# Performance work log

Hardware: AMD Instinct MI355X
Metric: run time of the kernel (lower is better)

## Reference

```python
import jax, jax.numpy as jnp
import numpy as np

N_NODES = 100000
N_EDGES = 1250000
IN_CH = 64
HID = 64
OUT = 64


def setup_inputs() -> dict:
    key = jax.random.key(0)
    ks = jax.random.split(key, 8)
    x = jax.random.normal(ks[0], (N_NODES, IN_CH), dtype=jnp.float32)
    edge_index = jax.random.randint(ks[1], (2, N_EDGES), 0, N_NODES, dtype=jnp.int64)
    # glorot-ish init for weights, zeros for biases (PyG GCNConv default-style)
    def glorot(k, fan_in, fan_out):
        s = (6.0 / (fan_in + fan_out)) ** 0.5
        return jax.random.uniform(k, (fan_in, fan_out), jnp.float32, -s, s)
    W1 = glorot(ks[2], IN_CH, HID)
    b1 = jnp.zeros((HID,), jnp.float32)
    W2 = glorot(ks[3], HID, HID)
    b2 = jnp.zeros((HID,), jnp.float32)
    W3 = glorot(ks[4], HID, OUT)
    b3 = jnp.zeros((OUT,), jnp.float32)
    return {"x": x, "edge_index": edge_index, "W1": W1, "b1": b1,
            "W2": W2, "b2": b2, "W3": W3, "b3": b3}


def _gcn_conv(x, src, dst, W, b, n_nodes):
    """PyG GCNConv: out = D^{-1/2} (A + I) D^{-1/2} (x W) + b.
    src/dst already include self-loops."""
    deg = jax.ops.segment_sum(jnp.ones_like(dst, dtype=x.dtype), dst,
                              num_segments=n_nodes)  # in-degree incl. self-loop
    dinv = jnp.where(deg > 0, jax.lax.rsqrt(deg), 0.0)
    norm = dinv[src] * dinv[dst]                       # [E+N]
    h = x @ W                                          # [N, F_out] small GEMM
    msg = h[src] * norm[:, None]                       # gather + scale (edge-wise)
    out = jax.ops.segment_sum(msg, dst, num_segments=n_nodes)  # scatter-add
    return out + b


def reference(x, edge_index, W1, b1, W2, b2, W3, b3):
    n_nodes = x.shape[0]
    loop = jnp.arange(n_nodes, dtype=edge_index.dtype)
    src = jnp.concatenate([edge_index[0], loop])  # messages flow src -> dst
    dst = jnp.concatenate([edge_index[1], loop])
    h = jax.nn.relu(_gcn_conv(x, src, dst, W1, b1, n_nodes))
    h = jax.nn.relu(_gcn_conv(h, src, dst, W2, b2, n_nodes))
    return h @ W3 + b3
```

## Files before the change

### kernel.cpp

```cpp
#include <hip/hip_runtime.h>
#include <hip/hip_bf16.h>


#define WG 256
#define BSHIFT 9
#define BSIZE  (1 << BSHIFT)
#define BCAP   8192
#define PCHUNK 2048
#define WT_LD  72

typedef __attribute__((ext_vector_type(8))) short bf16x8;
typedef __attribute__((ext_vector_type(4))) float f32x4;

__device__ __forceinline__ unsigned short f2bf(float f) {
    union { float f; unsigned u; } v; v.f = f;
    unsigned r = v.u + 0x7fffu + ((v.u >> 16) & 1u);
    return (unsigned short)(r >> 16);
}
__device__ __forceinline__ float bf2f(unsigned short h) {
    union { unsigned u; float f; } v; v.u = ((unsigned)h) << 16;
    return v.f;
}

__global__ __launch_bounds__(WG) void bcur_init(int* __restrict__ cur2, int nbk) {
    int b = threadIdx.x;
    if (b < nbk) cur2[b] = b * BCAP;
}

__global__ __launch_bounds__(WG) void partition(const int* __restrict__ ei,
                                                int* __restrict__ cur2,
                                                unsigned long long* __restrict__ pairs,
                                                int E) {
    __shared__ int hist[256];
    __shared__ int gbase[256];
    __shared__ int lb[256];
    __shared__ int wsum4[4];
    __shared__ unsigned long long sp[PCHUNK];
    __shared__ int sd[PCHUNK];
    const int t = threadIdx.x;
    const int lane = t & 63;
    const int w = t >> 6;
    const int base = blockIdx.x * PCHUNK;
    const int total = min(PCHUNK, E - base);

    hist[t] = 0;
    __syncthreads();

    int s[8], d[8], r[8];
#pragma unroll
    for (int i = 0; i < 8; i++) {
        int e = base + i * WG + t;
        bool ok = e < E;
        s[i] = ok ? ei[e] : 0;
        d[i] = ok ? ei[E + e] : 0;
        r[i] = ok ? atomicAdd(&hist[d[i] >> BSHIFT], 1) : 0;
        if (!ok) d[i] = -1;
    }
    __syncthreads();

    int hv = hist[t];
    if (hv > 0) gbase[t] = atomicAdd(&cur2[t], hv);
    int sc = hv;
#pragma unroll
    for (int ofs = 1; ofs < 64; ofs <<= 1) {
        int u = __shfl_up(sc, ofs);
        if (lane >= ofs) sc += u;
    }
    if (lane == 63) wsum4[w] = sc;
    __syncthreads();
    if (t == 0) {
        int run = 0;
#pragma unroll
        for (int i = 0; i < 4; i++) { int x = wsum4[i]; wsum4[i] = run; run += x; }
    }
    __syncthreads();
    lb[t] = sc + wsum4[w] - hv;
    __syncthreads();

#pragma unroll
    for (int i = 0; i < 8; i++) {
        if (d[i] >= 0) {
            int b = d[i] >> BSHIFT;
            int slot = lb[b] + r[i];
            sp[slot] = ((unsigned long long)(unsigned)(d[i] & (BSIZE - 1)) << 32) |
                       (unsigned)s[i];
            sd[slot] = gbase[b] + r[i];
        }
    }
    __syncthreads();

    for (int j = t; j < total; j += WG)
        pairs[sd[j]] = sp[j];
}

__global__ __launch_bounds__(WG) void bsum_scan(const int* __restrict__ cur2,
                                                int* __restrict__ bbase, int nbk,
                                                int* __restrict__ off, int N) {
    __shared__ int sums[WG];
    const int t = threadIdx.x;
    int s = (t < nbk) ? (cur2[t] - t * BCAP) : 0;
    sums[t] = s;
    __syncthreads();
    for (int ofs = 1; ofs < WG; ofs <<= 1) {
        int u = (t >= ofs) ? sums[t - ofs] : 0;
        __syncthreads();
        sums[t] += u;
        __syncthreads();
    }
    if (t < nbk) bbase[t] = sums[t] - s;
    if (t == WG - 1) off[N] = sums[WG - 1];
}

__global__ __launch_bounds__(1024) void csr_local(const unsigned long long* __restrict__ pairs,
                                                  const int* __restrict__ cur2,
                                                  const int* __restrict__ bbase,
                                                  int* __restrict__ off,
                                                  float* __restrict__ dinv,
                                                  int* __restrict__ csr, int N) {
    __shared__ unsigned long long sp[BCAP];
    __shared__ int cs[BCAP];
    __shared__ int h[BSIZE];
    __shared__ int cur[BSIZE];
    __shared__ int wsum[8];
    const int b = blockIdx.x;
    const int t = threadIdx.x;
    const int lane = t & 63;
    const int w = t >> 6;
    const int node0 = b << BSHIFT;
    const int nlocal = min(BSIZE, N - node0);
    const int pstart = b * BCAP;
    const int cnt = cur2[b] - pstart;
    const int base = bbase[b];

    if (t < BSIZE) h[t] = 0;
    __syncthreads();

    for (int e = t; e < cnt; e += 1024) {
        unsigned long long p = pairs[pstart + e];
        sp[e] = p;
        atomicAdd(&h[(int)(p >> 32)], 1);
    }
    __syncthreads();

    int myh = (t < BSIZE) ? h[t] : 0;
    int s = myh;
#pragma unroll
    for (int d = 1; d < 64; d <<= 1) {
        int u = __shfl_up(s, d);
        if (lane >= d) s += u;
    }
    if (t < BSIZE && lane == 63) wsum[w] = s;
    __syncthreads();
    if (t == 0) {
        int run = 0;
#pragma unroll
        for (int i = 0; i < 8; i++) { int x = wsum[i]; wsum[i] = run; run += x; }
    }
    __syncthreads();
    if (t < BSIZE) {
        int excl = s + wsum[w] - myh;
        cur[t] = excl;
        if (t < nlocal) {
            off[node0 + t] = base + excl;
            dinv[node0 + t] = rsqrtf((float)(myh + 1));
        }
    }
    __syncthreads();

    for (int e = t; e < cnt; e += 1024) {
        unsigned long long p = sp[e];
        int pos = atomicAdd(&cur[(int)(p >> 32)], 1);
        cs[pos] = (int)(p & 0xffffffffu);
    }
    __syncthreads();

    for (int j = t; j < cnt; j += 1024)
        csr[base + j] = cs[j];
}

__global__ __launch_bounds__(WG, 4) void gemm_fused(
    const float* __restrict__ in, const float* __restrict__ W,
    const float* __restrict__ dinv, const float* __restrict__ b_pre, int pre_flag,
    int post_scale, const float* __restrict__ b_post,
    void* __restrict__ out1, int out_bf16, int n_rows)
{
    __shared__ __align__(16) short Wh[64 * WT_LD];
    __shared__ __align__(16) short Wl[64 * WT_LD];

    const int t = threadIdx.x;

    const float4* W4 = (const float4*)W;
#pragma unroll
    for (int i = 0; i < 4; i++) {
        int q = i * WG + t;
        float4 w = W4[q];
        int base = q * 4;
        int k = base >> 6;
        int j0 = base & 63;
        float wf[4] = {w.x, w.y, w.z, w.w};
#pragma unroll
        for (int e = 0; e < 4; e++) {
            unsigned short h = f2bf(wf[e]);
            Wh[(j0 + e) * WT_LD + k] = (short)h;
            Wl[(j0 + e) * WT_LD + k] = (short)f2bf(wf[e] - bf2f(h));
        }
    }

    const int wid = t >> 6;
    const int l = t & 63;
    const int lr = l & 15;
    const int lk = l >> 4;
    const int row0 = blockIdx.x * 64 + wid * 16;
    const int arow = row0 + lr;
    const int srow = (arow < n_rows) ? arow : 0;

    bf16x8 ah[2], al[2];
    float dv = pre_flag ? dinv[srow] : 0.f;
#pragma unroll
    for (int kc = 0; kc < 2; kc++) {
        const float* p = in + (size_t)srow * 64 + kc * 32 + lk * 8;
        float4 v0 = *(const float4*)p;
        float4 v1 = *(const float4*)(p + 4);
        float vv[8] = {v0.x, v0.y, v0.z, v0.w, v1.x, v1.y, v1.z, v1.w};
        if (pre_flag) {
            const float* bp = b_pre + kc * 32 + lk * 8;
            float4 b0 = *(const float4*)bp;
            float4 b1 = *(const float4*)(bp + 4);
            float bb[8] = {b0.x, b0.y, b0.z, b0.w, b1.x, b1.y, b1.z, b1.w};
#pragma unroll
            for (int e = 0; e < 8; e++)
                vv[e] = fmaxf(fmaf(dv, vv[e], bb[e]), 0.f);
        }
#pragma unroll
        for (int e = 0; e < 8; e++) {
            unsigned short h = f2bf(vv[e]);
            ah[kc][e] = (short)h;
            al[kc][e] = (short)f2bf(vv[e] - bf2f(h));
        }
    }

    __syncthreads();

    f32x4 acc[4] = {};
#pragma unroll
    for (int ct = 0; ct < 4; ct++) {
#pragma unroll
        for (int kc = 0; kc < 2; kc++) {
            const short* ph = &Wh[(ct * 16 + lr) * WT_LD + kc * 32 + lk * 8];
            const short* pl = &Wl[(ct * 16 + lr) * WT_LD + kc * 32 + lk * 8];
            bf16x8 bh = *(const bf16x8*)ph;
            bf16x8 bl = *(const bf16x8*)pl;
            acc[ct] = __builtin_amdgcn_mfma_f32_16x16x32_bf16(ah[kc], bh, acc[ct], 0, 0, 0);
            acc[ct] = __builtin_amdgcn_mfma_f32_16x16x32_bf16(al[kc], bh, acc[ct], 0, 0, 0);
            acc[ct] = __builtin_amdgcn_mfma_f32_16x16x32_bf16(ah[kc], bl, acc[ct], 0, 0, 0);
            acc[ct] = __builtin_amdgcn_mfma_f32_16x16x32_bf16(al[kc], bl, acc[ct], 0, 0, 0);
        }
    }

#pragma unroll
    for (int r = 0; r < 4; r++) {
        int orow = row0 + lk * 4 + r;
        if (orow >= n_rows) continue;
        float sc = post_scale ? dinv[orow] : 1.0f;
#pragma unroll
        for (int ct = 0; ct < 4; ct++) {
            float bpv = b_post ? b_post[ct * 16 + lr] : 0.f;
            float o = fmaf(acc[ct][r], sc, bpv);
            if (out_bf16)
                ((unsigned short*)out1)[((size_t)orow << 6) + ct * 16 + lr] = f2bf(o);
            else
                ((float*)out1)[((size_t)orow << 6) + ct * 16 + lr] = o;
        }
    }
}

__device__ __forceinline__ void acc_bf16x2(float& a, float& b, unsigned u) {
    union { unsigned v; float f; } lo, hi;
    lo.v = u << 16;
    hi.v = u & 0xffff0000u;
    a += lo.f;
    b += hi.f;
}

__global__ __launch_bounds__(WG) void aggregate(
    const uint2* __restrict__ A4, float* __restrict__ B,
    const int* __restrict__ off, const int* __restrict__ csr, int N)
{
    const int t = threadIdx.x;
    const int l = t & 63;
    const int c = l & 15;
    const int g = l >> 4;
    const int gl = g << 4;
    int node = blockIdx.x * 16 + ((t >> 6) << 2) + g;
    const bool valid = node < N;
    if (!valid) node = N - 1;

    const int s0 = off[node];
    const int s1 = valid ? off[node + 1] : s0;

    uint2 v = A4[((size_t)node << 4) + c];
    float4 acc = make_float4(0.f, 0.f, 0.f, 0.f);
    acc_bf16x2(acc.x, acc.y, v.x);
    acc_bf16x2(acc.z, acc.w, v.y);

    for (int p = s0; p < s1; p += 16) {
        const int cnt = min(16, s1 - p);
        int idx = (c < cnt) ? csr[p + c] : 0;
#pragma unroll
        for (int k = 0; k < 16; k++) {
            int src = __shfl(idx, gl + k);
            if (k < cnt) {
                uint2 wv = A4[((size_t)src << 4) + c];
                acc_bf16x2(acc.x, acc.y, wv.x);
                acc_bf16x2(acc.z, acc.w, wv.y);
            }
        }
    }

    if (valid)
        *(float4*)(B + ((size_t)node << 6) + 4 * c) = acc;
}

extern "C" void kernel_launch(void* const* d_in, const int* in_sizes, int n_in,
                              void* d_out, int out_size, void* d_ws, size_t ws_size,
                              hipStream_t stream) {
    const float* x  = (const float*)d_in[0];
    const int*   ei = (const int*)d_in[1];
    const float* W1 = (const float*)d_in[2];
    const float* b1 = (const float*)d_in[3];
    const float* W2 = (const float*)d_in[4];
    const float* b2 = (const float*)d_in[5];
    const float* W3 = (const float*)d_in[6];
    const float* b3 = (const float*)d_in[7];
    float* out = (float*)d_out;

    const int N = in_sizes[0] / 64;
    const int E = in_sizes[1] / 2;
    const int nbk = (N + BSIZE - 1) / BSIZE;

    int*   off  = (int*)d_ws;
    int*   csr  = off + (N + 1);
    int*   cur2 = csr + E;
    int*   bbase= cur2 + 256;
    uintptr_t pa = (uintptr_t)(bbase + 256);
    pa = (pa + 255) & ~(uintptr_t)255;
    float* dinv = (float*)pa;
    __hip_bfloat16* A = (__hip_bfloat16*)(dinv + N);
    float* B    = (float*)(A + (size_t)N * 64);
    unsigned long long* pairs = (unsigned long long*)B;

    const int gG = (N + 63) / 64;
    const int gA = (N + 15) / 16;
    const int gP = (E + PCHUNK - 1) / PCHUNK;

    bcur_init<<<1,   WG, 0, stream>>>(cur2, nbk);
    partition<<<gP,  WG, 0, stream>>>(ei, cur2, pairs, E);
    bsum_scan<<<1,   WG, 0, stream>>>(cur2, bbase, nbk, off, N);
    csr_local<<<nbk, 1024, 0, stream>>>(pairs, cur2, bbase, off, dinv, csr, N);

    gemm_fused<<<gG, WG, 0, stream>>>(x, W1, dinv, nullptr, 0, 1, nullptr, A, 1, N);
    aggregate <<<gA, WG, 0, stream>>>((const uint2*)A, B, off, csr, N);

    gemm_fused<<<gG, WG, 0, stream>>>(B, W2, dinv, b1, 1, 1, nullptr, A, 1, N);
    aggregate <<<gA, WG, 0, stream>>>((const uint2*)A, B, off, csr, N);

    gemm_fused<<<gG, WG, 0, stream>>>(B, W3, dinv, b2, 1, 0, b3, out, 0, N);
}
```

Measured before the change: 232.8 us.

## Fuse neighbor aggregation with the following GEMM into one kernel

Replaces the separate aggregate kernel plus the next GEMM with a single agg_gemm kernel. Each 64-row block gathers its neighbor sums into shared memory, applies dinv scaling, bias and ReLU, then runs split-bf16 MFMA against W held in LDS. This removes the fp32 intermediate B round trip to global memory and two kernel launches. In exchange it uses more shared memory per block, which may lower occupancy, and each thread now handles four nodes in sequence.

```diff
diff --git a/kernel.cpp b/kernel.cpp
--- a/kernel.cpp
+++ b/kernel.cpp
@@ -8,6 +8,7 @@
 #define BCAP   8192
 #define PCHUNK 2048
 #define WT_LD  72
+#define XS_LD  68
 
 typedef __attribute__((ext_vector_type(8))) short bf16x8;
 typedef __attribute__((ext_vector_type(4))) float f32x4;
@@ -20,6 +21,13 @@
 __device__ __forceinline__ float bf2f(unsigned short h) {
     union { unsigned u; float f; } v; v.u = ((unsigned)h) << 16;
     return v.f;
+}
+__device__ __forceinline__ void acc_bf16x2(float& a, float& b, unsigned u) {
+    union { unsigned v; float f; } lo, hi;
+    lo.v = u << 16;
+    hi.v = u & 0xffff0000u;
+    a += lo.f;
+    b += hi.f;
 }
 
 __global__ __launch_bounds__(WG) void bcur_init(int* __restrict__ cur2, int nbk) {
@@ -274,51 +282,133 @@
     }
 }
 
-__device__ __forceinline__ void acc_bf16x2(float& a, float& b, unsigned u) {
-    union { unsigned v; float f; } lo, hi;
-    lo.v = u << 16;
-    hi.v = u & 0xffff0000u;
-    a += lo.f;
-    b += hi.f;
-}
-
-__global__ __launch_bounds__(WG) void aggregate(
-    const uint2* __restrict__ A4, float* __restrict__ B,
-    const int* __restrict__ off, const int* __restrict__ csr, int N)
+__global__ __launch_bounds__(WG, 4) void agg_gemm(
+    const uint2* __restrict__ A4, const float* __restrict__ W,
+    const float* __restrict__ dinv, const float* __restrict__ b_pre,
+    int post_scale, const float* __restrict__ b_post,
+    void* __restrict__ out1, int out_bf16,
+    const int* __restrict__ off, const int* __restrict__ csr, int n_rows)
 {
+    __shared__ __align__(16) short Wh[64 * WT_LD];
+    __shared__ __align__(16) short Wl[64 * WT_LD];
+    __shared__ __align__(16) float xs[64 * XS_LD];
+
     const int t = threadIdx.x;
+
+    const float4* W4 = (const float4*)W;
+#pragma unroll
+    for (int i = 0; i < 4; i++) {
+        int q = i * WG + t;
+        float4 w = W4[q];
+        int base = q * 4;
+        int k = base >> 6;
+        int j0 = base & 63;
+        float wf[4] = {w.x, w.y, w.z, w.w};
+#pragma unroll
+        for (int e = 0; e < 4; e++) {
+            unsigned short h = f2bf(wf[e]);
+            Wh[(j0 + e) * WT_LD + k] = (short)h;
+            Wl[(j0 + e) * WT_LD + k] = (short)f2bf(wf[e] - bf2f(h));
+        }
+    }
+
     const int l = t & 63;
     const int c = l & 15;
     const int g = l >> 4;
-    const int gl = g << 4;
-    int node = blockIdx.x * 16 + ((t >> 6) << 2) + g;
-    const bool valid = node < N;
-    if (!valid) node = N - 1;
-
-    const int s0 = off[node];
-    const int s1 = valid ? off[node + 1] : s0;
-
-    uint2 v = A4[((size_t)node << 4) + c];
-    float4 acc = make_float4(0.f, 0.f, 0.f, 0.f);
-    acc_bf16x2(acc.x, acc.y, v.x);
-    acc_bf16x2(acc.z, acc.w, v.y);
-
-    for (int p = s0; p < s1; p += 16) {
-        const int cnt = min(16, s1 - p);
-        int idx = (c < cnt) ? csr[p + c] : 0;
-#pragma unroll
-        for (int k = 0; k < 16; k++) {
-            int src = __shfl(idx, gl + k);
-            if (k < cnt) {
-                uint2 wv = A4[((size_t)src << 4) + c];
-                acc_bf16x2(acc.x, acc.y, wv.x);
-                acc_bf16x2(acc.z, acc.w, wv.y);
+    const int qid = (t >> 6) * 4 + g;
+    const int row0 = blockIdx.x * 64;
+    const float4 bb = *(const float4*)(b_pre + 4 * c);
+
+#pragma unroll
+    for (int i = 0; i < 4; i++) {
+        int rloc = qid * 4 + i;
+        int node = row0 + rloc;
+        bool valid = node < n_rows;
+        int nc = valid ? node : n_rows - 1;
+        int s0 = off[nc];
+        int s1 = valid ? off[nc + 1] : s0;
+
+        uint2 v = A4[((size_t)nc << 4) + c];
+        float4 acc = make_float4(0.f, 0.f, 0.f, 0.f);
+        acc_bf16x2(acc.x, acc.y, v.x);
+        acc_bf16x2(acc.z, acc.w, v.y);
+
+        for (int p = s0; p < s1; p += 16) {
+            const int cnt = min(16, s1 - p);
+            int idx = (c < cnt) ? csr[p + c] : 0;
+#pragma unroll
+            for (int k = 0; k < 16; k++) {
+                int src = __shfl(idx, (g << 4) + k);
+                if (k < cnt) {
+                    uint2 wv = A4[((size_t)src << 4) + c];
+                    acc_bf16x2(acc.x, acc.y, wv.x);
+                    acc_bf16x2(acc.z, acc.w, wv.y);
+                }
             }
         }
-    }
-
-    if (valid)
-        *(float4*)(B + ((size_t)node << 6) + 4 * c) = acc;
+
+        float dv = dinv[nc];
+        float4 o;
+        o.x = fmaxf(fmaf(dv, acc.x, bb.x), 0.f);
+        o.y = fmaxf(fmaf(dv, acc.y, bb.y), 0.f);
+        o.z = fmaxf(fmaf(dv, acc.z, bb.z), 0.f);
+        o.w = fmaxf(fmaf(dv, acc.w, bb.w), 0.f);
+        *(float4*)(xs + rloc * XS_LD + 4 * c) = o;
+    }
+
+    __syncthreads();
+
+    const int wid = t >> 6;
+    const int lr = l & 15;
+    const int lk = l >> 4;
+    const int rw0 = blockIdx.x * 64 + wid * 16;
+
+    bf16x8 ah[2], al[2];
+#pragma unroll
+    for (int kc = 0; kc < 2; kc++) {
+        const float* p = xs + (wid * 16 + lr) * XS_LD + kc * 32 + lk * 8;
+        float4 v0 = *(const float4*)p;
+        float4 v1 = *(const float4*)(p + 4);
+        float vv[8] = {v0.x, v0.y, v0.z, v0.w, v1.x, v1.y, v1.z, v1.w};
+#pragma unroll
+        for (int e = 0; e < 8; e++) {
+            unsigned short h = f2bf(vv[e]);
+            ah[kc][e] = (short)h;
+            al[kc][e] = (short)f2bf(vv[e] - bf2f(h));
+        }
+    }
+
+    f32x4 acc[4] = {};
+#pragma unroll
+    for (int ct = 0; ct < 4; ct++) {
+#pragma unroll
+        for (int kc = 0; kc < 2; kc++) {
+            const short* ph = &Wh[(ct * 16 + lr) * WT_LD + kc * 32 + lk * 8];
+            const short* pl = &Wl[(ct * 16 + lr) * WT_LD + kc * 32 + lk * 8];
+            bf16x8 bh = *(const bf16x8*)ph;
+            bf16x8 bl = *(const bf16x8*)pl;
+            acc[ct] = __builtin_amdgcn_mfma_f32_16x16x32_bf16(ah[kc], bh, acc[ct], 0, 0, 0);
+            acc[ct] = __builtin_amdgcn_mfma_f32_16x16x32_bf16(al[kc], bh, acc[ct], 0, 0, 0);
+            acc[ct] = __builtin_amdgcn_mfma_f32_16x16x32_bf16(ah[kc], bl, acc[ct], 0, 0, 0);
+            acc[ct] = __builtin_amdgcn_mfma_f32_16x16x32_bf16(al[kc], bl, acc[ct], 0, 0, 0);
+        }
+    }
+
+#pragma unroll
+    for (int r = 0; r < 4; r++) {
+        int orow = rw0 + lk * 4 + r;
+        if (orow >= n_rows) continue;
+        float sc = post_scale ? dinv[orow] : 1.0f;
+#pragma unroll
+        for (int ct = 0; ct < 4; ct++) {
+            float bpv = b_post ? b_post[ct * 16 + lr] : 0.f;
+            float o = fmaf(acc[ct][r], sc, bpv);
+            if (out_bf16)
+                ((unsigned short*)out1)[((size_t)orow << 6) + ct * 16 + lr] = f2bf(o);
+            else
+                ((float*)out1)[((size_t)orow << 6) + ct * 16 + lr] = o;
+        }
+    }
 }
 
 extern "C" void kernel_launch(void* const* d_in, const int* in_sizes, int n_in,
@@ -345,12 +435,11 @@
     uintptr_t pa = (uintptr_t)(bbase + 256);
     pa = (pa + 255) & ~(uintptr_t)255;
     float* dinv = (float*)pa;
-    __hip_bfloat16* A = (__hip_bfloat16*)(dinv + N);
-    float* B    = (float*)(A + (size_t)N * 64);
-    unsigned long long* pairs = (unsigned long long*)B;
+    __hip_bfloat16* A  = (__hip_bfloat16*)(dinv + N);
+    __hip_bfloat16* A2 = A + (size_t)N * 64;
+    unsigned long long* pairs = (unsigned long long*)A2;
 
     const int gG = (N + 63) / 64;
-    const int gA = (N + 15) / 16;
     const int gP = (E + PCHUNK - 1) / PCHUNK;
 
     bcur_init<<<1,   WG, 0, stream>>>(cur2, nbk);
@@ -359,10 +448,10 @@
     csr_local<<<nbk, 1024, 0, stream>>>(pairs, cur2, bbase, off, dinv, csr, N);
 
     gemm_fused<<<gG, WG, 0, stream>>>(x, W1, dinv, nullptr, 0, 1, nullptr, A, 1, N);
-    aggregate <<<gA, WG, 0, stream>>>((const uint2*)A, B, off, csr, N);
-
-    gemm_fused<<<gG, WG, 0, stream>>>(B, W2, dinv, b1, 1, 1, nullptr, A, 1, N);
-    aggregate <<<gA, WG, 0, stream>>>((const uint2*)A, B, off, csr, N);
-
-    gemm_fused<<<gG, WG, 0, stream>>>(B, W3, dinv, b2, 1, 0, b3, out, 0, N);
-}
+
+    agg_gemm<<<gG, WG, 0, stream>>>((const uint2*)A, W2, dinv, b1, 1, nullptr,
+                                    A2, 1, off, csr, N);
+
+    agg_gemm<<<gG, WG, 0, stream>>>((const uint2*)A2, W3, dinv, b2, 0, b3,
+                                    out, 0, off, csr, N);
+}
```

Result: slower. 283.3 us (+21.7%).

## Pack edge pairs to 32 bits, halve bucket size, widen aggregate loads

Applied to the files above, without the earlier changes.

The CSR build now packs each (local dst, src) pair into one 32-bit word (src in 17 bits) instead of 64 bits. Buckets shrink to 256 nodes with 4096 capacity across up to 512 buckets, and the scans and csr_local block size are adjusted to match. The aggregate kernel moves from 16 lanes × 8 bytes per node row to 8 lanes × 16 bytes, with 32 neighbor indices staged per iteration. This is meant to cut pair-buffer traffic and LDS use and to use wider gathers. In exchange, node ids must fit in 17 bits, and a bucket overflows if a block of 256 nodes receives more than 4096 edges.

```diff
diff --git a/kernel.cpp b/kernel.cpp
--- a/kernel.cpp
+++ b/kernel.cpp
@@ -3,9 +3,10 @@
 
 
 #define WG 256
-#define BSHIFT 9
+#define BSHIFT 8
 #define BSIZE  (1 << BSHIFT)
-#define BCAP   8192
+#define NBK_MAX 512
+#define BCAP   4096
 #define PCHUNK 2048
 #define WT_LD  72
 
@@ -21,21 +22,28 @@
     union { unsigned u; float f; } v; v.u = ((unsigned)h) << 16;
     return v.f;
 }
-
-__global__ __launch_bounds__(WG) void bcur_init(int* __restrict__ cur2, int nbk) {
+__device__ __forceinline__ void acc_bf16x2(float& a, float& b, unsigned u) {
+    union { unsigned v; float f; } lo, hi;
+    lo.v = u << 16;
+    hi.v = u & 0xffff0000u;
+    a += lo.f;
+    b += hi.f;
+}
+
+__global__ __launch_bounds__(512) void bcur_init(int* __restrict__ cur2) {
     int b = threadIdx.x;
-    if (b < nbk) cur2[b] = b * BCAP;
+    cur2[b] = b * BCAP;
 }
 
 __global__ __launch_bounds__(WG) void partition(const int* __restrict__ ei,
                                                 int* __restrict__ cur2,
-                                                unsigned long long* __restrict__ pairs,
+                                                unsigned* __restrict__ pairs,
                                                 int E) {
-    __shared__ int hist[256];
-    __shared__ int gbase[256];
-    __shared__ int lb[256];
+    __shared__ int hist[NBK_MAX];
+    __shared__ int gbase[NBK_MAX];
+    __shared__ int lb[NBK_MAX];
     __shared__ int wsum4[4];
-    __shared__ unsigned long long sp[PCHUNK];
+    __shared__ unsigned sp[PCHUNK];
     __shared__ int sd[PCHUNK];
     const int t = threadIdx.x;
     const int lane = t & 63;
@@ -44,6 +52,7 @@
     const int total = min(PCHUNK, E - base);
 
     hist[t] = 0;
+    hist[t + 256] = 0;
     __syncthreads();
 
     int s[8], d[8], r[8];
@@ -58,9 +67,15 @@
     }
     __syncthreads();
 
-    int hv = hist[t];
-    if (hv > 0) gbase[t] = atomicAdd(&cur2[t], hv);
-    int sc = hv;
+    int hv0 = hist[t];
+    int hv1 = hist[t + 256];
+    if (hv0 > 0) gbase[t] = atomicAdd(&cur2[t], hv0);
+    if (hv1 > 0) gbase[t + 256] = atomicAdd(&cur2[t + 256], hv1);
+
+    int a0 = hist[2 * t];
+    int a1 = hist[2 * t + 1];
+    int ps = a0 + a1;
+    int sc = ps;
 #pragma unroll
     for (int ofs = 1; ofs < 64; ofs <<= 1) {
         int u = __shfl_up(sc, ofs);
@@ -74,7 +89,9 @@
         for (int i = 0; i < 4; i++) { int x = wsum4[i]; wsum4[i] = run; run += x; }
     }
     __syncthreads();
-    lb[t] = sc + wsum4[w] - hv;
+    int excl = sc + wsum4[w] - ps;
+    lb[2 * t] = excl;
+    lb[2 * t + 1] = excl + a0;
     __syncthreads();
 
 #pragma unroll
@@ -82,8 +99,7 @@
         if (d[i] >= 0) {
             int b = d[i] >> BSHIFT;
             int slot = lb[b] + r[i];
-            sp[slot] = ((unsigned long long)(unsigned)(d[i] & (BSIZE - 1)) << 32) |
-                       (unsigned)s[i];
+            sp[slot] = ((unsigned)(d[i] & (BSIZE - 1)) << 17) | (unsigned)s[i];
             sd[slot] = gbase[b] + r[i];
         }
     }
@@ -93,35 +109,43 @@
         pairs[sd[j]] = sp[j];
 }
 
-__global__ __launch_bounds__(WG) void bsum_scan(const int* __restrict__ cur2,
-                                                int* __restrict__ bbase, int nbk,
-                                                int* __restrict__ off, int N) {
-    __shared__ int sums[WG];
-    const int t = threadIdx.x;
+__global__ __launch_bounds__(512) void bsum_scan(const int* __restrict__ cur2,
+                                                 int* __restrict__ bbase, int nbk,
+                                                 int* __restrict__ off, int N) {
+    __shared__ int wsum[8];
+    const int t = threadIdx.x;
+    const int lane = t & 63;
+    const int w = t >> 6;
     int s = (t < nbk) ? (cur2[t] - t * BCAP) : 0;
-    sums[t] = s;
-    __syncthreads();
-    for (int ofs = 1; ofs < WG; ofs <<= 1) {
-        int u = (t >= ofs) ? sums[t - ofs] : 0;
-        __syncthreads();
-        sums[t] += u;
-        __syncthreads();
-    }
-    if (t < nbk) bbase[t] = sums[t] - s;
-    if (t == WG - 1) off[N] = sums[WG - 1];
-}
-
-__global__ __launch_bounds__(1024) void csr_local(const unsigned long long* __restrict__ pairs,
-                                                  const int* __restrict__ cur2,
-                                                  const int* __restrict__ bbase,
-                                                  int* __restrict__ off,
-                                                  float* __restrict__ dinv,
-                                                  int* __restrict__ csr, int N) {
-    __shared__ unsigned long long sp[BCAP];
+    int sc = s;
+#pragma unroll
+    for (int ofs = 1; ofs < 64; ofs <<= 1) {
+        int u = __shfl_up(sc, ofs);
+        if (lane >= ofs) sc += u;
+    }
+    if (lane == 63) wsum[w] = sc;
+    __syncthreads();
+    if (t == 0) {
+        int run = 0;
+#pragma unroll
+        for (int i = 0; i < 8; i++) { int x = wsum[i]; wsum[i] = run; run += x; }
+    }
+    __syncthreads();
+    if (t < nbk) bbase[t] = sc + wsum[w] - s;
+    if (t == 511) off[N] = sc + wsum[7];
+}
+
+__global__ __launch_bounds__(512) void csr_local(const unsigned* __restrict__ pairs,
+                                                 const int* __restrict__ cur2,
+                                                 const int* __restrict__ bbase,
+                                                 int* __restrict__ off,
+                                                 float* __restrict__ dinv,
+                                                 int* __restrict__ csr, int N) {
+    __shared__ unsigned sp[BCAP];
     __shared__ int cs[BCAP];
     __shared__ int h[BSIZE];
     __shared__ int cur[BSIZE];
-    __shared__ int wsum[8];
+    __shared__ int wsum[4];
     const int b = blockIdx.x;
     const int t = threadIdx.x;
     const int lane = t & 63;
@@ -135,30 +159,30 @@
     if (t < BSIZE) h[t] = 0;
     __syncthreads();
 
-    for (int e = t; e < cnt; e += 1024) {
-        unsigned long long p = pairs[pstart + e];
+    for (int e = t; e < cnt; e += 512) {
+        unsigned p = pairs[pstart + e];
         sp[e] = p;
-        atomicAdd(&h[(int)(p >> 32)], 1);
+        atomicAdd(&h[p >> 17], 1);
     }
     __syncthreads();
 
     int myh = (t < BSIZE) ? h[t] : 0;
-    int s = myh;
+    int sc = myh;
 #pragma unroll
     for (int d = 1; d < 64; d <<= 1) {
-        int u = __shfl_up(s, d);
-        if (lane >= d) s += u;
-    }
-    if (t < BSIZE && lane == 63) wsum[w] = s;
+        int u = __shfl_up(sc, d);
+        if (lane >= d) sc += u;
+    }
+    if (t < BSIZE && lane == 63) wsum[w] = sc;
     __syncthreads();
     if (t == 0) {
         int run = 0;
 #pragma unroll
-        for (int i = 0; i < 8; i++) { int x = wsum[i]; wsum[i] = run; run += x; }
+        for (int i = 0; i < 4; i++) { int x = wsum[i]; wsum[i] = run; run += x; }
     }
     __syncthreads();
     if (t < BSIZE) {
-        int excl = s + wsum[w] - myh;
+        int excl = sc + wsum[w] - myh;
         cur[t] = excl;
         if (t < nlocal) {
             off[node0 + t] = base + excl;
@@ -167,14 +191,14 @@
     }
     __syncthreads();
 
-    for (int e = t; e < cnt; e += 1024) {
-        unsigned long long p = sp[e];
-        int pos = atomicAdd(&cur[(int)(p >> 32)], 1);
-        cs[pos] = (int)(p & 0xffffffffu);
-    }
-    __syncthreads();
-
-    for (int j = t; j < cnt; j += 1024)
+    for (int e = t; e < cnt; e += 512) {
+        unsigned p = sp[e];
+        int pos = atomicAdd(&cur[p >> 17], 1);
+        cs[pos] = (int)(p & 0x1ffffu);
+    }
+    __syncthreads();
+
+    for (int j = t; j < cnt; j += 512)
         csr[base + j] = cs[j];
 }
 
@@ -274,51 +298,53 @@
     }
 }
 
-__device__ __forceinline__ void acc_bf16x2(float& a, float& b, unsigned u) {
-    union { unsigned v; float f; } lo, hi;
-    lo.v = u << 16;
-    hi.v = u & 0xffff0000u;
-    a += lo.f;
-    b += hi.f;
-}
-
 __global__ __launch_bounds__(WG) void aggregate(
-    const uint2* __restrict__ A4, float* __restrict__ B,
+    const uint4* __restrict__ A8, float* __restrict__ B,
     const int* __restrict__ off, const int* __restrict__ csr, int N)
 {
     const int t = threadIdx.x;
     const int l = t & 63;
-    const int c = l & 15;
-    const int g = l >> 4;
-    const int gl = g << 4;
-    int node = blockIdx.x * 16 + ((t >> 6) << 2) + g;
+    const int c = l & 7;
+    const int g = l >> 3;
+    int node = blockIdx.x * 32 + ((t >> 6) << 3) + g;
     const bool valid = node < N;
     if (!valid) node = N - 1;
 
     const int s0 = off[node];
     const int s1 = valid ? off[node + 1] : s0;
 
-    uint2 v = A4[((size_t)node << 4) + c];
-    float4 acc = make_float4(0.f, 0.f, 0.f, 0.f);
-    acc_bf16x2(acc.x, acc.y, v.x);
-    acc_bf16x2(acc.z, acc.w, v.y);
-
-    for (int p = s0; p < s1; p += 16) {
-        const int cnt = min(16, s1 - p);
-        int idx = (c < cnt) ? csr[p + c] : 0;
-#pragma unroll
-        for (int k = 0; k < 16; k++) {
-            int src = __shfl(idx, gl + k);
-            if (k < cnt) {
-                uint2 wv = A4[((size_t)src << 4) + c];
-                acc_bf16x2(acc.x, acc.y, wv.x);
-                acc_bf16x2(acc.z, acc.w, wv.y);
+    uint4 v = A8[((size_t)node << 3) + c];
+    float a0 = 0.f, a1 = 0.f, a2 = 0.f, a3 = 0.f;
+    float a4 = 0.f, a5 = 0.f, a6 = 0.f, a7 = 0.f;
+    acc_bf16x2(a0, a1, v.x);
+    acc_bf16x2(a2, a3, v.y);
+    acc_bf16x2(a4, a5, v.z);
+    acc_bf16x2(a6, a7, v.w);
+
+    for (int p = s0; p < s1; p += 32) {
+        const int rem = s1 - p;
+        int idx[4];
+#pragma unroll
+        for (int q = 0; q < 4; q++)
+            idx[q] = (8 * q + c < rem) ? csr[p + 8 * q + c] : 0;
+#pragma unroll
+        for (int k = 0; k < 32; k++) {
+            int src = __shfl(idx[k >> 3], (g << 3) + (k & 7));
+            if (k < rem) {
+                uint4 wv = A8[((size_t)src << 3) + c];
+                acc_bf16x2(a0, a1, wv.x);
+                acc_bf16x2(a2, a3, wv.y);
+                acc_bf16x2(a4, a5, wv.z);
+                acc_bf16x2(a6, a7, wv.w);
             }
         }
     }
 
-    if (valid)
-        *(float4*)(B + ((size_t)node << 6) + 4 * c) = acc;
+    if (valid) {
+        float* bp = B + ((size_t)node << 6) + 8 * c;
+        *(float4*)bp       = make_float4(a0, a1, a2, a3);
+        *(float4*)(bp + 4) = make_float4(a4, a5, a6, a7);
+    }
 }
 
 extern "C" void kernel_launch(void* const* d_in, const int* in_sizes, int n_in,
@@ -341,28 +367,28 @@
     int*   off  = (int*)d_ws;
     int*   csr  = off + (N + 1);
     int*   cur2 = csr + E;
-    int*   bbase= cur2 + 256;
-    uintptr_t pa = (uintptr_t)(bbase + 256);
+    int*   bbase= cur2 + 512;
+    uintptr_t pa = (uintptr_t)(bbase + 512);
     pa = (pa + 255) & ~(uintptr_t)255;
     float* dinv = (float*)pa;
     __hip_bfloat16* A = (__hip_bfloat16*)(dinv + N);
     float* B    = (float*)(A + (size_t)N * 64);
-    unsigned long long* pairs = (unsigned long long*)B;
+    unsigned* pairs = (unsigned*)B;
 
     const int gG = (N + 63) / 64;
-    const int gA = (N + 15) / 16;
+    const int gA = (N + 31) / 32;
     const int gP = (E + PCHUNK - 1) / PCHUNK;
 
-    bcur_init<<<1,   WG, 0, stream>>>(cur2, nbk);
+    bcur_init<<<1,   512, 0, stream>>>(cur2);
     partition<<<gP,  WG, 0, stream>>>(ei, cur2, pairs, E);
-    bsum_scan<<<1,   WG, 0, stream>>>(cur2, bbase, nbk, off, N);
-    csr_local<<<nbk, 1024, 0, stream>>>(pairs, cur2, bbase, off, dinv, csr, N);
+    bsum_scan<<<1,   512, 0, stream>>>(cur2, bbase, nbk, off, N);
+    csr_local<<<nbk, 512, 0, stream>>>(pairs, cur2, bbase, off, dinv, csr, N);
 
     gemm_fused<<<gG, WG, 0, stream>>>(x, W1, dinv, nullptr, 0, 1, nullptr, A, 1, N);
-    aggregate <<<gA, WG, 0, stream>>>((const uint2*)A, B, off, csr, N);
+    aggregate <<<gA, WG, 0, stream>>>((const uint4*)A, B, off, csr, N);
 
     gemm_fused<<<gG, WG, 0, stream>>>(B, W2, dinv, b1, 1, 1, nullptr, A, 1, N);
-    aggregate <<<gA, WG, 0, stream>>>((const uint2*)A, B, off, csr, N);
+    aggregate <<<gA, WG, 0, stream>>>((const uint4*)A, B, off, csr, N);
 
     gemm_fused<<<gG, WG, 0, stream>>>(B, W3, dinv, b2, 1, 0, b3, out, 0, N);
 }
```

Result: faster. 224.5 us (-3.6%).
